# Performance work log

Measured on AMD Instinct MI355X. Metric: run time of the kernel, lower is better.

## Reference

```python
import jax, jax.numpy as jnp
import numpy as np
from jax.scipy.linalg import solve_triangular

EMB = 2048; NKH = 16; NVH = 32; DK = 128; DV = 128
KSZ = 4; EPS = 1e-6; CHUNK = 64
KEY_DIM = NKH * DK; VAL_DIM = NVH * DV
CONV_DIM = 2 * KEY_DIM + VAL_DIM  # q,k (key_dim each) + v (value_dim)
B, S = 1, 4096  # S % CHUNK == 0 -> no padding path


def setup_inputs() -> dict:
    key = jax.random.key(0)
    ks = jax.random.split(key, 7)
    s = 0.02
    return {
        "hidden_states": jax.random.normal(ks[0], (B, S, EMB), jnp.float32),
        "W_qkvz": jax.random.normal(ks[1], (EMB, 2 * KEY_DIM + 2 * VAL_DIM), jnp.float32) * s,
        "W_ba": jax.random.normal(ks[2], (EMB, 2 * NVH), jnp.float32) * s,
        "conv_kernel": jax.random.normal(ks[3], (KSZ, 1, CONV_DIM), jnp.float32) * 0.1,
        "A_log": jnp.log(jax.random.uniform(ks[4], (NVH,), jnp.float32, 1e-9, 16.0)),
        "dt_bias": jnp.ones((NVH,), jnp.float32),
        "norm_weight": jnp.ones((DV,), jnp.float32),
        "W_out": jax.random.normal(ks[5], (VAL_DIM, EMB), jnp.float32) * s,
    }


def _chunk_gated_delta_rule(q, k, v, g, beta):
    """q,k: [B,S,H,DK]; v: [B,S,H,DV]; g,beta: [B,S,H]. Returns [B,S,H,DV]."""
    dt = q.dtype
    prec = jax.lax.Precision.HIGHEST
    q = jnp.transpose(q, (0, 2, 1, 3)).astype(jnp.float32)
    k = jnp.transpose(k, (0, 2, 1, 3)).astype(jnp.float32)
    v = jnp.transpose(v, (0, 2, 1, 3)).astype(jnp.float32)
    beta = jnp.transpose(beta, (0, 2, 1)).astype(jnp.float32)
    g = jnp.transpose(g, (0, 2, 1)).astype(jnp.float32)
    b, h, s, dk = k.shape
    dv = v.shape[-1]
    nc = s // CHUNK
    q = q * jax.lax.rsqrt(jnp.float32(dk))
    v_beta = v * beta[..., None]
    k_beta = k * beta[..., None]
    qc = q.reshape(b, h, nc, CHUNK, dk)
    kc = k.reshape(b, h, nc, CHUNK, dk)
    kbc = k_beta.reshape(b, h, nc, CHUNK, dk)
    vbc = v_beta.reshape(b, h, nc, CHUNK, dv)
    gc = g.reshape(b, h, nc, CHUNK)
    g_cum = jnp.cumsum(gc, axis=-1)                        # [b,h,nc,C]
    g_diff = g_cum[..., :, None] - g_cum[..., None, :]     # [b,h,nc,C,C]
    decay = jnp.exp(jnp.tril(g_diff))
    tri_incl = jnp.triu(jnp.ones((CHUNK, CHUNK), bool), k=0)
    L = -jnp.matmul(kbc, jnp.swapaxes(kc, -1, -2), precision=prec) * decay
    L = jnp.where(tri_incl, 0.0, L)  # strictly lower
    eye = jnp.eye(CHUNK, dtype=jnp.float32)
    # UT transform: original fori_loop forward-substitution == (I - L)^{-1}
    attn = solve_triangular(eye - L, jnp.broadcast_to(eye, L.shape), lower=True)
    v_intra = jnp.matmul(attn, vbc, precision=prec)
    k_cumdecay = jnp.matmul(attn, kbc * jnp.exp(g_cum)[..., None], precision=prec)
    state0 = jnp.zeros((b, h, dk, dv), jnp.float32)
    tri_strict = jnp.triu(jnp.ones((CHUNK, CHUNK), bool), k=1)
    xs = tuple(jnp.moveaxis(t, 2, 0) for t in (qc, kc, v_intra, k_cumdecay, g_cum, decay))

    def scan_body(state, x):
        q_i, k_i, v_i, kcd_i, g_i, dm_i = x
        a_i = jnp.matmul(q_i, jnp.swapaxes(k_i, -1, -2), precision=prec) * dm_i
        a_i = jnp.where(tri_strict, 0.0, a_i)
        v_new = v_i - jnp.matmul(kcd_i, state, precision=prec)
        out_i = jnp.matmul(q_i * jnp.exp(g_i)[..., None], state, precision=prec) \
              + jnp.matmul(a_i, v_new, precision=prec)
        g_last = g_i[..., -1]
        new_state = state * jnp.exp(g_last)[..., None, None] \
            + jnp.matmul(jnp.swapaxes(k_i * jnp.exp(g_last[..., None] - g_i)[..., None], -1, -2),
                         v_new, precision=prec)
        return new_state, out_i

    _, out = jax.lax.scan(scan_body, state0, xs)
    out = jnp.moveaxis(out, 0, 2).reshape(b, h, s, dv)
    return jnp.transpose(out, (0, 2, 1, 3)).astype(dt)


def reference(hidden_states, W_qkvz, W_ba, conv_kernel, A_log, dt_bias, norm_weight, W_out):
    b, s, _ = hidden_states.shape
    vk = NVH // NKH  # v heads per k head
    qkvz = hidden_states @ W_qkvz                          # [b,s,12288]
    ba = hidden_states @ W_ba                              # [b,s,64]
    mixed = qkvz.reshape(b, s, NKH, 2 * DK + 2 * vk * DV)
    q, k, v_raw, z_raw = jnp.split(mixed, [DK, 2 * DK, 2 * DK + vk * DV], axis=3)
    value = v_raw.reshape(b, s, NVH, DV)
    z = z_raw.reshape(b, s, NVH, DV)
    mixed_ba = ba.reshape(b, s, NKH, 2 * vk)
    b_raw, a_raw = jnp.split(mixed_ba, [vk], axis=3)
    b_gate = b_raw.reshape(b, s, NVH)
    a_gate = a_raw.reshape(b, s, NVH)
    # depthwise causal conv over the concatenated q,k,v channels
    qkv = jnp.concatenate([q.reshape(b, s, -1), k.reshape(b, s, -1), value.reshape(b, s, -1)], axis=-1)
    x = jnp.pad(qkv, ((0, 0), (KSZ - 1, 0), (0, 0)))
    conv = jax.lax.conv_general_dilated(x, conv_kernel, (1,), 'VALID',
                                        dimension_numbers=('NWC', 'WIO', 'NWC'),
                                        feature_group_count=CONV_DIM)
    qkv_c = jax.nn.silu(conv.astype(jnp.float32)).astype(hidden_states.dtype)
    q_c, k_c, v_c = jnp.split(qkv_c, [KEY_DIM, 2 * KEY_DIM], axis=-1)
    query = q_c.reshape(b, s, NKH, DK)
    key = k_c.reshape(b, s, NKH, DK)
    value = v_c.reshape(b, s, NVH, DV)
    beta = jax.nn.sigmoid(b_gate)
    g = (-jnp.exp(A_log.astype(jnp.float32))
         * jax.nn.softplus(a_gate.astype(jnp.float32) + dt_bias.astype(jnp.float32))
         ).astype(hidden_states.dtype)
    query = jnp.repeat(query, vk, axis=2)
    key = jnp.repeat(key, vk, axis=2)
    core = _chunk_gated_delta_rule(query, key, value, g, beta)  # [b,s,NVH,DV]
    # gated RMSNorm (Mamba2-style): gate first, then normalize
    xf = core.astype(jnp.float32) * jax.nn.silu(z.astype(jnp.float32))
    var = jnp.mean(xf * xf, axis=-1, keepdims=True)
    xf = xf * jax.lax.rsqrt(var + EPS) * norm_weight
    out = xf.astype(hidden_states.dtype).reshape(b, s, VAL_DIM)
    return out @ W_out
```

## Files before the change

kernel.cpp:

```cpp
#include <hip/hip_runtime.h>


typedef __attribute__((ext_vector_type(8))) __bf16 bf16x8;
typedef __attribute__((ext_vector_type(4))) float f32x4;
typedef __bf16 bf16_t;

#define MFMA_BF16(A, B, C) __builtin_amdgcn_mfma_f32_16x16x32_bf16((A), (B), (C), 0, 0, 0)

__device__ __forceinline__ void async16(const bf16_t* g, bf16_t* l) {
  __builtin_amdgcn_global_load_lds(
      (const __attribute__((address_space(1))) unsigned*)g,
      (__attribute__((address_space(3))) unsigned*)l, 16, 0, 0);
}

__device__ __forceinline__ bf16_t f2bf(float x) {
  unsigned u = __builtin_bit_cast(unsigned, x);
  unsigned r = u + 0x7fffu + ((u >> 16) & 1u);
  unsigned short s = (unsigned short)(r >> 16);
  return __builtin_bit_cast(bf16_t, s);
}
__device__ __forceinline__ float bf2f(bf16_t b) {
  unsigned short s = __builtin_bit_cast(unsigned short, b);
  unsigned u = ((unsigned)s) << 16;
  return __builtin_bit_cast(float, u);
}
__device__ __forceinline__ unsigned packhl(float x) {
  bf16_t h = f2bf(x);
  bf16_t l = f2bf(x - bf2f(h));
  return (((unsigned)__builtin_bit_cast(unsigned short, h)) << 16) |
         (unsigned)__builtin_bit_cast(unsigned short, l);
}
__device__ __forceinline__ float upk(unsigned u) {
  return __builtin_bit_cast(float, u & 0xffff0000u) +
         __builtin_bit_cast(float, u << 16);
}

struct FragPair { bf16x8 hi, lo; };

__device__ __forceinline__ void load8(float v[8], const float* p) {
  float4 a = *(const float4*)p;
  float4 b = *(const float4*)(p + 4);
  v[0] = a.x; v[1] = a.y; v[2] = a.z; v[3] = a.w;
  v[4] = b.x; v[5] = b.y; v[6] = b.z; v[7] = b.w;
}
__device__ __forceinline__ void load8u(unsigned v[8], const unsigned* p) {
  uint4 a = *(const uint4*)p;
  uint4 b = *(const uint4*)(p + 4);
  v[0] = a.x; v[1] = a.y; v[2] = a.z; v[3] = a.w;
  v[4] = b.x; v[5] = b.y; v[6] = b.z; v[7] = b.w;
}
__device__ __forceinline__ FragPair split8(const float v[8]) {
  FragPair f;
#pragma unroll
  for (int j = 0; j < 8; j++) {
    bf16_t h = f2bf(v[j]);
    f.hi[j] = h;
    f.lo[j] = f2bf(v[j] - bf2f(h));
  }
  return f;
}
__device__ __forceinline__ FragPair unpack8(const unsigned v[8]) {
  FragPair f;
#pragma unroll
  for (int j = 0; j < 8; j++) {
    f.hi[j] = __builtin_bit_cast(bf16_t, (unsigned short)(v[j] >> 16));
    f.lo[j] = __builtin_bit_cast(bf16_t, (unsigned short)(v[j] & 0xffffu));
  }
  return f;
}

__global__ void k_cvt(const float* __restrict__ in, bf16_t* __restrict__ out, int n) {
  int i = (blockIdx.x * 256 + threadIdx.x) * 4;
  if (i + 3 < n) {
    float4 v = *(const float4*)(in + i);
    out[i + 0] = f2bf(v.x); out[i + 1] = f2bf(v.y);
    out[i + 2] = f2bf(v.z); out[i + 3] = f2bf(v.w);
  }
}

__global__ void k_transpose_cvt(const float* __restrict__ in, bf16_t* __restrict__ out,
                                int K, int N) {
  __shared__ bf16_t tile[64 * 65];
  int n0 = blockIdx.x * 64, k0 = blockIdx.y * 64;
  int c = threadIdx.x & 63, rg = threadIdx.x >> 6;
#pragma unroll
  for (int rr = 0; rr < 16; rr++) {
    int r = rr * 4 + rg;
    tile[c * 65 + r] = f2bf(in[(size_t)(k0 + r) * N + n0 + c]);
  }
  __syncthreads();
#pragma unroll
  for (int rr = 0; rr < 16; rr++) {
    int r = rr * 4 + rg;
    out[(size_t)(n0 + r) * K + k0 + c] = tile[r * 65 + c];
  }
}

__global__ void k_ktrans(const bf16_t* __restrict__ kb, bf16_t* __restrict__ kbT) {
  __shared__ __align__(16) bf16_t t[128][72];
  int kh = blockIdx.x >> 6, ci = blockIdx.x & 63, s0 = ci * 64;
  int s = threadIdx.x & 63, dg = threadIdx.x >> 6;
  const bf16_t* src = kb + (size_t)(s0 + s) * 2048 + kh * 128 + dg * 32;
#pragma unroll
  for (int j = 0; j < 4; j++) {
    bf16x8 v = *(const bf16x8*)(src + j * 8);
#pragma unroll
    for (int e = 0; e < 8; e++) t[dg * 32 + j * 8 + e][s] = v[e];
  }
  __syncthreads();
  int d = threadIdx.x >> 1, sh = (threadIdx.x & 1) * 32;
  bf16_t* dst = kbT + ((size_t)blockIdx.x * 128 + d) * 64 + sh;
#pragma unroll
  for (int j = 0; j < 4; j++)
    *(bf16x8*)(dst + j * 8) = *(const bf16x8*)(&t[d][sh + j * 8]);
}

__global__ __launch_bounds__(256) void k_gemm(const bf16_t* __restrict__ A,
                                              const bf16_t* __restrict__ BT,
                                              float* __restrict__ C, int M, int N, int K) {
  __shared__ __align__(16) bf16_t sA[128 * 32];
  __shared__ __align__(16) bf16_t sB[128 * 32];
  const int tid = threadIdx.x;
  const int lane = tid & 63, w = tid >> 6;
  const int quad = lane >> 4, l15 = lane & 15;
  const int m0 = blockIdx.y * 128, n0 = blockIdx.x * 128;
  const int wm = (w >> 1) * 64, wn = (w & 1) * 64;
  f32x4 acc[4][4];
#pragma unroll
  for (int a = 0; a < 4; a++)
#pragma unroll
    for (int b = 0; b < 4; b++) { f32x4 z = {0.f, 0.f, 0.f, 0.f}; acc[a][b] = z; }
  const int sb = (lane & 7) ^ ((lane >> 3) & 7);
  const int srow = ((tid >> 3) << 1) + (sb >> 2);
  const int scol = (sb & 3) * 8;
  const bf16_t* gA = A + (size_t)(m0 + srow) * K + scol;
  const bf16_t* gB = BT + (size_t)(n0 + srow) * K + scol;
  bf16_t* lA = sA + w * 512;
  bf16_t* lB = sB + w * 512;
  const int rh = l15 >> 1;
  const int bs = (((l15 & 1) << 2) + quad) ^ rh;
  const int foff = rh * 64 + bs * 8;
  for (int kt = 0; kt < K; kt += 32) {
    async16(gA + kt, lA);
    async16(gA + (size_t)64 * K + kt, lA + 2048);
    async16(gB + kt, lB);
    async16(gB + (size_t)64 * K + kt, lB + 2048);
    __syncthreads();
    bf16x8 af[4], bfv[4];
#pragma unroll
    for (int t = 0; t < 4; t++) {
      af[t]  = *(const bf16x8*)(sA + ((wm >> 1) + t * 8) * 64 + foff);
      bfv[t] = *(const bf16x8*)(sB + ((wn >> 1) + t * 8) * 64 + foff);
    }
#pragma unroll
    for (int mt = 0; mt < 4; mt++)
#pragma unroll
      for (int nt = 0; nt < 4; nt++)
        acc[mt][nt] = MFMA_BF16(af[mt], bfv[nt], acc[mt][nt]);
    __syncthreads();
  }
#pragma unroll
  for (int mt = 0; mt < 4; mt++)
#pragma unroll
    for (int nt = 0; nt < 4; nt++) {
      int row0 = m0 + wm + mt * 16 + quad * 4;
      int col = n0 + wn + nt * 16 + l15;
#pragma unroll
      for (int r = 0; r < 4; r++)
        C[(size_t)(row0 + r) * N + col] = acc[mt][nt][r];
    }
}

__global__ __launch_bounds__(512, 2) void k_gemm_qkvz(const bf16_t* __restrict__ A,
                                                      const bf16_t* __restrict__ BT,
                                                      bf16_t* __restrict__ qkvb,
                                                      bf16_t* __restrict__ zb,
                                                      int M, int N, int K) {
  __shared__ __align__(16) bf16_t sA[4 * 8192];
  __shared__ __align__(16) bf16_t sB[4 * 8192];
  const int tid = threadIdx.x;
  const int lane = tid & 63, w = tid >> 6;
  const int quad = lane >> 4, l15 = lane & 15;

  const int nwg = gridDim.x * gridDim.y;
  const int cpx = nwg >> 3;
  int id = blockIdx.y * gridDim.x + blockIdx.x;
  id = (id & 7) * cpx + (id >> 3);
  const int bx = id % gridDim.x, by = id / gridDim.x;
  const int m0 = by * 256, n0 = bx * 256;
  const int wm = (w >> 2) * 128, wn = (w & 3) * 64;

  f32x4 acc[8][4];
#pragma unroll
  for (int m = 0; m < 8; m++)
#pragma unroll
    for (int n = 0; n < 4; n++) { f32x4 z = {0.f, 0.f, 0.f, 0.f}; acc[m][n] = z; }

  const int srow = w * 16 + (lane >> 2);
  const int sq = (lane & 3) ^ ((lane >> 3) & 3);
  const bf16_t* gA = A + (size_t)(m0 + srow) * K + sq * 8;
  const bf16_t* gB = BT + (size_t)(n0 + srow) * K + sq * 8;
  const size_t rowskip = (size_t)128 * K;

  const int pblk = (quad ^ ((l15 >> 1) & 3)) << 3;
  const int fA = (wm + l15) * 32 + pblk;
  const int fB = (wn + l15) * 32 + pblk;

  const int NT = K >> 5;

  auto stage = [&](int t) {
    bf16_t* lA = sA + (t & 3) * 8192 + w * 512;
    bf16_t* lB = sB + (t & 3) * 8192 + w * 512;
    const bf16_t* pA = gA + t * 32;
    const bf16_t* pB = gB + t * 32;
    async16(pA, lA);
    async16(pA + rowskip, lA + 4096);
    async16(pB, lB);
    async16(pB + rowskip, lB + 4096);
  };

  if (0 < NT) stage(0);
  if (1 < NT) stage(1);
  if (2 < NT) stage(2);

  for (int t = 0; t < NT; ++t) {
    if (t + 3 < NT) stage(t + 3);
    const int ahead = NT - 1 - t;
    if (ahead >= 3)      asm volatile("s_waitcnt vmcnt(12)" ::: "memory");
    else if (ahead == 2) asm volatile("s_waitcnt vmcnt(8)" ::: "memory");
    else if (ahead == 1) asm volatile("s_waitcnt vmcnt(4)" ::: "memory");
    else                 asm volatile("s_waitcnt vmcnt(0)" ::: "memory");
    __builtin_amdgcn_s_barrier();
    asm volatile("" ::: "memory");
    __builtin_amdgcn_sched_barrier(0);

    const bf16_t* bA = sA + (t & 3) * 8192;
    const bf16_t* bB = sB + (t & 3) * 8192;
    bf16x8 af[8], bfv[4];
#pragma unroll
    for (int m = 0; m < 8; m++) af[m] = *(const bf16x8*)(bA + fA + m * 512);
#pragma unroll
    for (int n = 0; n < 4; n++) bfv[n] = *(const bf16x8*)(bB + fB + n * 512);

    __builtin_amdgcn_s_setprio(1);
#pragma unroll
    for (int m = 0; m < 8; m++)
#pragma unroll
      for (int n = 0; n < 4; n++)
        acc[m][n] = MFMA_BF16(af[m], bfv[n], acc[m][n]);
    __builtin_amdgcn_s_setprio(0);

    asm volatile("" ::: "memory");
    __builtin_amdgcn_sched_barrier(0);
    __builtin_amdgcn_s_barrier();
  }

#pragma unroll
  for (int n = 0; n < 4; n++) {
    int c = n0 + wn + n * 16 + l15;
    int kh = c / 768;
    int rr = c - kh * 768;
    bool isz = (rr >= 512);
    bf16_t* dst = isz ? zb : qkvb;
    size_t stride = isz ? 4096 : 8192;
    size_t coff = isz ? (size_t)(kh * 256 + (rr - 512)) : (size_t)(kh * 512 + rr);
#pragma unroll
    for (int m = 0; m < 8; m++) {
      int row0 = m0 + wm + m * 16 + quad * 4;
#pragma unroll
      for (int r = 0; r < 4; r++)
        dst[(size_t)(row0 + r) * stride + coff] = f2bf(acc[m][n][r]);
    }
  }
}

__global__ __launch_bounds__(256) void k_ba(const float* __restrict__ hs,
                                            const float* __restrict__ Wba,
                                            const float* __restrict__ A_log,
                                            const float* __restrict__ dtb,
                                            float* __restrict__ g, float* __restrict__ beta) {
  __shared__ float sH[4][2048];
  int s0 = blockIdx.x * 32;
  int c = threadIdx.x & 63, sg = threadIdx.x >> 6;
  for (int rg = 0; rg < 8; rg++) {
    __syncthreads();
    for (int i = threadIdx.x; i < 2048; i += 256) {
      int r = i >> 9, kk = (i & 511) * 4;
      *(float4*)(&sH[r][kk]) = *(const float4*)(hs + (size_t)(s0 + rg * 4 + r) * 2048 + kk);
    }
    __syncthreads();
    float dot = 0.f;
    for (int kk = 0; kk < 2048; kk += 4) {
      float4 hv = *(const float4*)(&sH[sg][kk]);
      dot += hv.x * Wba[(kk + 0) * 64 + c] + hv.y * Wba[(kk + 1) * 64 + c] +
             hv.z * Wba[(kk + 2) * 64 + c] + hv.w * Wba[(kk + 3) * 64 + c];
    }
    int s = s0 + rg * 4 + sg;
    int hh = c >> 2, j = c & 3;
    if (j < 2) {
      int vh = hh * 2 + j;
      beta[s * 32 + vh] = 1.f / (1.f + __expf(-dot));
    } else {
      int vh = hh * 2 + (j - 2);
      float x = dot + dtb[vh];
      float sp = (x > 20.f) ? x : log1pf(__expf(x));
      g[s * 32 + vh] = -__expf(A_log[vh]) * sp;
    }
  }
}

__global__ void k_conv(const bf16_t* __restrict__ qkvb, const float* __restrict__ ck,
                       bf16_t* __restrict__ qb, bf16_t* __restrict__ kb,
                       bf16_t* __restrict__ vb) {
  int c = blockIdx.x * 256 + threadIdx.x;
  int s0 = blockIdx.y * 128;
  int col, dstc, dstride;
  bf16_t* dst;
  float scale = 1.0f;
  if (c < 2048) {
    int hh = c >> 7, d = c & 127;
    col = hh * 512 + d; dst = qb; dstc = c; dstride = 2048;
    scale = 0.08838834764831845f;
  } else if (c < 4096) {
    int cc = c - 2048, hh = cc >> 7, d = cc & 127;
    col = hh * 512 + 128 + d; dst = kb; dstc = cc; dstride = 2048;
  } else {
    int cc = c - 4096, vh = cc >> 7, d = cc & 127;
    col = (vh >> 1) * 512 + 256 + (vh & 1) * 128 + d; dst = vb; dstc = cc; dstride = 4096;
  }
  float w0 = ck[c], w1 = ck[8192 + c], w2 = ck[2 * 8192 + c], w3 = ck[3 * 8192 + c];
  float x0 = 0.f, x1 = 0.f, x2 = 0.f;
  if (s0 >= 3) {
    x0 = bf2f(qkvb[(size_t)(s0 - 3) * 8192 + col]);
    x1 = bf2f(qkvb[(size_t)(s0 - 2) * 8192 + col]);
    x2 = bf2f(qkvb[(size_t)(s0 - 1) * 8192 + col]);
  }
  for (int s = s0; s < s0 + 128; s++) {
    float x3 = bf2f(qkvb[(size_t)s * 8192 + col]);
    float y = w0 * x0 + w1 * x1 + w2 * x2 + w3 * x3;
    y = y / (1.f + __expf(-y));
    dst[(size_t)s * dstride + dstc] = f2bf(y * scale);
    x0 = x1; x1 = x2; x2 = x3;
  }
}

__global__ __launch_bounds__(256) void k_phaseA(const bf16_t* __restrict__ kb,
                                                const bf16_t* __restrict__ vb,
                                                const float* __restrict__ g,
                                                const float* __restrict__ beta,
                                                float* __restrict__ vi,
                                                bf16_t* __restrict__ kcdn) {
  __shared__ __align__(16) char smem[36608];
  float* sGc = (float*)smem;
  float* sBt = (float*)(smem + 256);
  float* sBE = (float*)(smem + 512);
  float* sP  = (float*)(smem + 768);
  bf16_t* sQ  = (bf16_t*)(smem + 18176);
  bf16_t* sQT = (bf16_t*)(smem + 27392);
  bf16_t* sVT = (bf16_t*)(smem + 18176);
  bf16_t* sKT = (bf16_t*)(smem + 27392);

  const int tid = threadIdx.x, lane = tid & 63, w = tid >> 6;
  const int quad = lane >> 4, l15 = lane & 15;
  const int h = blockIdx.x >> 6, ci = blockIdx.x & 63;
  const int kh = h >> 1, s0 = ci * 64;
  const int m = w * 16 + l15;

  if (tid < 64) {
    float gv = g[(size_t)(s0 + tid) * 32 + h];
    float bv = beta[(size_t)(s0 + tid) * 32 + h];
#pragma unroll
    for (int off = 1; off < 64; off <<= 1) {
      float t = __shfl_up(gv, off, 64);
      if (tid >= off) gv += t;
    }
    sGc[tid] = gv; sBt[tid] = bv; sBE[tid] = bv * __expf(gv);
  }
  __syncthreads();

  const bf16_t* krow = kb + (size_t)s0 * 2048 + kh * 128;
  bf16x8 ak[4];
#pragma unroll
  for (int ks = 0; ks < 4; ks++)
    ak[ks] = *(const bf16x8*)(krow + (size_t)m * 2048 + ks * 32 + quad * 8);
  f32x4 accL[4];
#pragma unroll
  for (int nt = 0; nt < 4; nt++) { f32x4 z = {0.f, 0.f, 0.f, 0.f}; accL[nt] = z; }
#pragma unroll
  for (int nt = 0; nt < 4; nt++)
#pragma unroll
    for (int ks = 0; ks < 4; ks++) {
      bf16x8 bk = *(const bf16x8*)(krow + (size_t)(nt * 16 + l15) * 2048 + ks * 32 + quad * 8);
      accL[nt] = MFMA_BF16(ak[ks], bk, accL[nt]);
    }
#pragma unroll
  for (int nt = 0; nt < 4; nt++) {
    int j = nt * 16 + l15;
#pragma unroll
    for (int r = 0; r < 4; r++) {
      int i = w * 16 + quad * 4 + r;
      float Lij = (i > j) ? (-accL[nt][r] * sBt[i] * __expf(sGc[i] - sGc[j])) : 0.f;
      sP[i * 68 + j] = ((i == j) ? 1.f : 0.f) + Lij;
      bf16_t q16 = f2bf(Lij);
      sQ[i * 72 + j] = q16;
      sQT[j * 72 + i] = q16;
    }
  }
  __syncthreads();

  for (int it = 0; it < 5; it++) {
    f32x4 accQ[4];
#pragma unroll
    for (int nt = 0; nt < 4; nt++) { f32x4 z = {0.f, 0.f, 0.f, 0.f}; accQ[nt] = z; }
    bf16x8 qa[2];
#pragma unroll
    for (int ks = 0; ks < 2; ks++)
      qa[ks] = *(const bf16x8*)(sQ + m * 72 + ks * 32 + quad * 8);
#pragma unroll
    for (int nt = 0; nt < 4; nt++)
#pragma unroll
      for (int ks = 0; ks < 2; ks++) {
        bf16x8 qv = *(const bf16x8*)(sQT + (nt * 16 + l15) * 72 + ks * 32 + quad * 8);
        accQ[nt] = MFMA_BF16(qa[ks], qv, accQ[nt]);
      }
    __syncthreads();
#pragma unroll
    for (int nt = 0; nt < 4; nt++) {
      int j = nt * 16 + l15;
#pragma unroll
      for (int r = 0; r < 4; r++) {
        int i = w * 16 + quad * 4 + r;
        bf16_t q16 = f2bf(accQ[nt][r]);
        sQ[i * 72 + j] = q16;
        sQT[j * 72 + i] = q16;
      }
    }
    __syncthreads();
    f32x4 accP[4];
#pragma unroll
    for (int nt = 0; nt < 4; nt++) { f32x4 z = {0.f, 0.f, 0.f, 0.f}; accP[nt] = z; }
    FragPair pa[2];
#pragma unroll
    for (int ks = 0; ks < 2; ks++) {
      float v[8];
      load8(v, sP + m * 68 + ks * 32 + quad * 8);
      pa[ks] = split8(v);
    }
#pragma unroll
    for (int nt = 0; nt < 4; nt++)
#pragma unroll
      for (int ks = 0; ks < 2; ks++) {
        bf16x8 qv = *(const bf16x8*)(sQT + (nt * 16 + l15) * 72 + ks * 32 + quad * 8);
        accP[nt] = MFMA_BF16(pa[ks].hi, qv, accP[nt]);
        accP[nt] = MFMA_BF16(pa[ks].lo, qv, accP[nt]);
      }
#pragma unroll
    for (int nt = 0; nt < 4; nt++) {
      int j = nt * 16 + l15;
#pragma unroll
      for (int r = 0; r < 4; r++) {
        int i = w * 16 + quad * 4 + r;
        sP[i * 68 + j] += accP[nt][r];
      }
    }
  }

  FragPair paV[2], paK[2];
#pragma unroll
  for (int ks = 0; ks < 2; ks++) {
    float v[8];
    load8(v, sP + m * 68 + ks * 32 + quad * 8);
    float vv[8], vk[8];
#pragma unroll
    for (int jj = 0; jj < 8; jj++) {
      int i = ks * 32 + quad * 8 + jj;
      vv[jj] = v[jj] * sBt[i];
      vk[jj] = v[jj] * sBE[i];
    }
    paV[ks] = split8(vv);
    paK[ks] = split8(vk);
  }

  for (int hf = 0; hf < 2; hf++) {
    __syncthreads();
    {
      int sidx = tid & 63, dg = tid >> 6;
      const bf16_t* vsrc = vb + (size_t)(s0 + sidx) * 4096 + h * 128 + hf * 64 + dg * 16;
      const bf16_t* ksrc = kb + (size_t)(s0 + sidx) * 2048 + kh * 128 + hf * 64 + dg * 16;
      bf16x8 v0 = *(const bf16x8*)vsrc;
      bf16x8 v1 = *(const bf16x8*)(vsrc + 8);
      bf16x8 k0 = *(const bf16x8*)ksrc;
      bf16x8 k1 = *(const bf16x8*)(ksrc + 8);
#pragma unroll
      for (int e = 0; e < 8; e++) {
        sVT[(dg * 16 + e) * 72 + sidx] = v0[e];
        sVT[(dg * 16 + 8 + e) * 72 + sidx] = v1[e];
        sKT[(dg * 16 + e) * 72 + sidx] = k0[e];
        sKT[(dg * 16 + 8 + e) * 72 + sidx] = k1[e];
      }
    }
    __syncthreads();
    f32x4 accV[4], accK[4];
#pragma unroll
    for (int nt = 0; nt < 4; nt++) {
      f32x4 z = {0.f, 0.f, 0.f, 0.f};
      accV[nt] = z; accK[nt] = z;
    }
#pragma unroll
    for (int nt = 0; nt < 4; nt++)
#pragma unroll
      for (int ks = 0; ks < 2; ks++) {
        bf16x8 bv = *(const bf16x8*)(sVT + (nt * 16 + l15) * 72 + ks * 32 + quad * 8);
        accV[nt] = MFMA_BF16(paV[ks].hi, bv, accV[nt]);
        accV[nt] = MFMA_BF16(paV[ks].lo, bv, accV[nt]);
        bf16x8 bk = *(const bf16x8*)(sKT + (nt * 16 + l15) * 72 + ks * 32 + quad * 8);
        accK[nt] = MFMA_BF16(paK[ks].hi, bk, accK[nt]);
        accK[nt] = MFMA_BF16(paK[ks].lo, bk, accK[nt]);
      }
#pragma unroll
    for (int nt = 0; nt < 4; nt++) {
      int col = hf * 64 + nt * 16 + l15;
#pragma unroll
      for (int r = 0; r < 4; r++) {
        int row = w * 16 + quad * 4 + r;
        size_t o = ((size_t)h * 4096 + s0 + row) * 128 + col;
        vi[o] = accV[nt][r];
        kcdn[o] = f2bf(-accK[nt][r]);
      }
    }
  }
}

__global__ __launch_bounds__(256) void k_phaseB(const bf16_t* __restrict__ qb,
                                                const bf16_t* __restrict__ kbT,
                                                const float* __restrict__ g,
                                                const float* __restrict__ vi,
                                                const bf16_t* __restrict__ kcdn,
                                                bf16_t* __restrict__ vnT,
                                                bf16_t* __restrict__ outp) {
  __shared__ __align__(16) char smem[13312];
  float* sGc2 = (float*)smem;
  unsigned* sSTp = (unsigned*)(smem + 512);
  unsigned* sVTp = (unsigned*)(smem + 8960);
  const int tid = threadIdx.x, lane = tid & 63, w = tid >> 6;
  const int quad = lane >> 4, l15 = lane & 15;
  const int h = blockIdx.x >> 3, cg = blockIdx.x & 7;
  const int kh = h >> 1, col0 = cg * 16;
  const int m = w * 16 + l15;

  for (int i = tid; i < 16 * 132; i += 256) sSTp[i] = 0u;
  if (tid < 64) {
    float gv = g[(size_t)tid * 32 + h];
#pragma unroll
    for (int off = 1; off < 64; off <<= 1) {
      float t = __shfl_up(gv, off, 64);
      if (tid >= off) gv += t;
    }
    sGc2[tid] = gv;
  }
  __syncthreads();

  for (int ci = 0; ci < 64; ci++) {
    const int s0 = ci * 64;
    const float* sGc = sGc2 + (ci & 1) * 64;

    const bf16_t* kcrow = kcdn + ((size_t)h * 4096 + s0 + m) * 128;
    const bf16_t* qrow = qb + (size_t)(s0 + m) * 2048 + kh * 128;
    bf16x8 a1[4], a2[4], kT[2][2];
#pragma unroll
    for (int d = 0; d < 4; d++) {
      a1[d] = *(const bf16x8*)(kcrow + d * 32 + quad * 8);
      a2[d] = *(const bf16x8*)(qrow + d * 32 + quad * 8);
    }
#pragma unroll
    for (int mi = 0; mi < 2; mi++)
#pragma unroll
      for (int ks = 0; ks < 2; ks++)
        kT[mi][ks] = *(const bf16x8*)(kbT + ((size_t)(kh * 64 + ci) * 128 +
                                             w * 32 + mi * 16 + l15) * 64 + ks * 32 + quad * 8);
    const int colg = col0 + l15;
    size_t vbase = ((size_t)h * 4096 + s0 + w * 16 + quad * 4) * 128 + colg;
    f32x4 accV = {vi[vbase], vi[vbase + 128], vi[vbase + 256], vi[vbase + 384]};
    f32x4 accO = {0.f, 0.f, 0.f, 0.f};
#pragma unroll
    for (int d = 0; d < 4; d++) {
      unsigned u[8];
      load8u(u, sSTp + l15 * 132 + d * 32 + quad * 8);
      FragPair B = unpack8(u);
      accV = MFMA_BF16(a1[d], B.hi, accV);
      accV = MFMA_BF16(a1[d], B.lo, accV);
      accO = MFMA_BF16(a2[d], B.hi, accO);
      accO = MFMA_BF16(a2[d], B.lo, accO);
    }
    const float gl = sGc[63];
    {
      bf16_t* vout = vnT + ((size_t)(h * 64 + ci) * 128 + colg) * 64 + w * 16 + quad * 4;
      bf16_t* oout = outp + vbase;
      ushort4 vv;
      unsigned pk[4];
      unsigned short vb_[4];
#pragma unroll
      for (int r = 0; r < 4; r++) {
        float gr = sGc[w * 16 + quad * 4 + r];
        oout[(size_t)r * 128] = f2bf(accO[r] * __expf(gr));
        vb_[r] = __builtin_bit_cast(unsigned short, f2bf(accV[r]));
        pk[r] = packhl(accV[r] * __expf(gl - gr));
      }
      vv.x = vb_[0]; vv.y = vb_[1]; vv.z = vb_[2]; vv.w = vb_[3];
      *(ushort4*)vout = vv;
      uint4 pv; pv.x = pk[0]; pv.y = pk[1]; pv.z = pk[2]; pv.w = pk[3];
      *(uint4*)(sVTp + l15 * 68 + w * 16 + quad * 4) = pv;
    }
    __syncthreads();

    f32x4 accD[2];
#pragma unroll
    for (int mi = 0; mi < 2; mi++) { f32x4 z = {0.f, 0.f, 0.f, 0.f}; accD[mi] = z; }
#pragma unroll
    for (int ks = 0; ks < 2; ks++) {
      unsigned u[8];
      load8u(u, sVTp + l15 * 68 + ks * 32 + quad * 8);
      FragPair Bv = unpack8(u);
#pragma unroll
      for (int mi = 0; mi < 2; mi++) {
        accD[mi] = MFMA_BF16(kT[mi][ks], Bv.hi, accD[mi]);
        accD[mi] = MFMA_BF16(kT[mi][ks], Bv.lo, accD[mi]);
      }
    }
    float egl = __expf(gl);
#pragma unroll
    for (int mi = 0; mi < 2; mi++) {
      int row0 = w * 32 + mi * 16 + quad * 4;
      unsigned* ps = sSTp + l15 * 132 + row0;
      uint4 old4 = *(uint4*)ps;
      uint4 nu;
      nu.x = packhl(upk(old4.x) * egl + accD[mi][0]);
      nu.y = packhl(upk(old4.y) * egl + accD[mi][1]);
      nu.z = packhl(upk(old4.z) * egl + accD[mi][2]);
      nu.w = packhl(upk(old4.w) * egl + accD[mi][3]);
      *(uint4*)ps = nu;
    }
    if (ci + 1 < 64 && tid < 64) {
      float gv = g[(size_t)((ci + 1) * 64 + tid) * 32 + h];
#pragma unroll
      for (int off = 1; off < 64; off <<= 1) {
        float t = __shfl_up(gv, off, 64);
        if (tid >= off) gv += t;
      }
      sGc2[((ci + 1) & 1) * 64 + tid] = gv;
    }
    __syncthreads();
  }
}

__global__ __launch_bounds__(256) void k_phaseC(const bf16_t* __restrict__ qb,
                                                const bf16_t* __restrict__ kb,
                                                const float* __restrict__ g,
                                                const bf16_t* __restrict__ vnT,
                                                const bf16_t* __restrict__ outp,
                                                const bf16_t* __restrict__ zb,
                                                const float* __restrict__ nw,
                                                bf16_t* __restrict__ xf) {
  __shared__ __align__(16) char smem[17664];
  float* sGc = (float*)smem;
  unsigned* sAp = (unsigned*)(smem + 256);
  const int tid = threadIdx.x, lane = tid & 63, w = tid >> 6;
  const int quad = lane >> 4, l15 = lane & 15;
  const int h = blockIdx.x >> 6, ci = blockIdx.x & 63;
  const int kh = h >> 1, s0 = ci * 64;
  const int m = w * 16 + l15;

  if (tid < 64) {
    float gv = g[(size_t)(s0 + tid) * 32 + h];
#pragma unroll
    for (int off = 1; off < 64; off <<= 1) {
      float t = __shfl_up(gv, off, 64);
      if (tid >= off) gv += t;
    }
    sGc[tid] = gv;
  }
  __syncthreads();

  const bf16_t* qrow = qb + (size_t)s0 * 2048 + kh * 128;
  const bf16_t* krow = kb + (size_t)s0 * 2048 + kh * 128;
  bf16x8 aq[4];
#pragma unroll
  for (int ks = 0; ks < 4; ks++)
    aq[ks] = *(const bf16x8*)(qrow + (size_t)m * 2048 + ks * 32 + quad * 8);
  f32x4 accA[4];
#pragma unroll
  for (int nt = 0; nt < 4; nt++) { f32x4 z = {0.f, 0.f, 0.f, 0.f}; accA[nt] = z; }
#pragma unroll
  for (int nt = 0; nt < 4; nt++)
#pragma unroll
    for (int ks = 0; ks < 4; ks++) {
      bf16x8 bk = *(const bf16x8*)(krow + (size_t)(nt * 16 + l15) * 2048 + ks * 32 + quad * 8);
      accA[nt] = MFMA_BF16(aq[ks], bk, accA[nt]);
    }
#pragma unroll
  for (int nt = 0; nt < 4; nt++) {
    int j = nt * 16 + l15;
#pragma unroll
    for (int r = 0; r < 4; r++) {
      int i = w * 16 + quad * 4 + r;
      float a = (i >= j) ? accA[nt][r] * __expf(sGc[i] - sGc[j]) : 0.f;
      sAp[i * 68 + j] = packhl(a);
    }
  }
  __syncthreads();

  FragPair Aa[2];
#pragma unroll
  for (int ks = 0; ks < 2; ks++) {
    unsigned u[8];
    load8u(u, sAp + m * 68 + ks * 32 + quad * 8);
    Aa[ks] = unpack8(u);
  }
  f32x4 accO[8];
#pragma unroll
  for (int nt = 0; nt < 8; nt++) {
    size_t base = ((size_t)h * 4096 + s0 + w * 16 + quad * 4) * 128 + nt * 16 + l15;
    f32x4 z;
    z[0] = bf2f(outp[base]); z[1] = bf2f(outp[base + 128]);
    z[2] = bf2f(outp[base + 256]); z[3] = bf2f(outp[base + 384]);
    accO[nt] = z;
  }
#pragma unroll
  for (int nt = 0; nt < 8; nt++)
#pragma unroll
    for (int ks = 0; ks < 2; ks++) {
      bf16x8 bv = *(const bf16x8*)(vnT + ((size_t)(h * 64 + ci) * 128 + nt * 16 + l15) * 64 +
                                   ks * 32 + quad * 8);
      accO[nt] = MFMA_BF16(Aa[ks].hi, bv, accO[nt]);
      accO[nt] = MFMA_BF16(Aa[ks].lo, bv, accO[nt]);
    }

  float xv[8][4];
  float ss[4] = {0.f, 0.f, 0.f, 0.f};
#pragma unroll
  for (int nt = 0; nt < 8; nt++) {
    int dv = nt * 16 + l15;
#pragma unroll
    for (int r = 0; r < 4; r++) {
      int s = s0 + w * 16 + quad * 4 + r;
      float z = bf2f(zb[(size_t)s * 4096 + h * 128 + dv]);
      float gate = z / (1.f + __expf(-z));
      float val = accO[nt][r] * gate;
      xv[nt][r] = val;
      ss[r] += val * val;
    }
  }
#pragma unroll
  for (int off = 1; off < 16; off <<= 1) {
#pragma unroll
    for (int r = 0; r < 4; r++) ss[r] += __shfl_xor(ss[r], off, 64);
  }
  float rs[4];
#pragma unroll
  for (int r = 0; r < 4; r++) rs[r] = rsqrtf(ss[r] * (1.f / 128.f) + 1e-6f);
#pragma unroll
  for (int nt = 0; nt < 8; nt++) {
    int dv = nt * 16 + l15;
    float nwv = nw[dv];
#pragma unroll
    for (int r = 0; r < 4; r++) {
      int s = s0 + w * 16 + quad * 4 + r;
      xf[(size_t)s * 4096 + h * 128 + dv] = f2bf(xv[nt][r] * rs[r] * nwv);
    }
  }
}

extern "C" void kernel_launch(void* const* d_in, const int* in_sizes, int n_in,
                              void* d_out, int out_size, void* d_ws, size_t ws_size,
                              hipStream_t stream) {
  const float* hs = (const float*)d_in[0];
  const float* Wqkvz = (const float*)d_in[1];
  const float* Wba = (const float*)d_in[2];
  const float* convk = (const float*)d_in[3];
  const float* A_log = (const float*)d_in[4];
  const float* dtb = (const float*)d_in[5];
  const float* nw = (const float*)d_in[6];
  const float* Wout = (const float*)d_in[7];
  float* out = (float*)d_out;
  char* ws = (char*)d_ws;

  const size_t NEED = 252706816u;
  if (ws_size < NEED) return;

  bf16_t* hsbf = (bf16_t*)(ws + 0);
  bf16_t* wqkT = (bf16_t*)(ws + 16777216);
  bf16_t* qb   = (bf16_t*)(ws + 0);
  bf16_t* kb   = (bf16_t*)(ws + 16777216);
  bf16_t* vb   = (bf16_t*)(ws + 33554432);
  bf16_t* vnT  = (bf16_t*)(ws + 33554432);
  bf16_t* qkvb = (bf16_t*)(ws + 67108864);
  float*  vi   = (float*)(ws + 67108864);
  bf16_t* xf   = (bf16_t*)(ws + 67108864);
  bf16_t* zb   = (bf16_t*)(ws + 134217728);
  float*  gbuf = (float*)(ws + 167772160);
  float*  bbuf = (float*)(ws + 168296448);
  bf16_t* kcdn = (bf16_t*)(ws + 168820736);
  bf16_t* woutT= (bf16_t*)(ws + 168820736);
  bf16_t* outp = (bf16_t*)(ws + 202375168);
  bf16_t* kbT  = (bf16_t*)(ws + 235929600);

  k_cvt<<<8192, 256, 0, stream>>>(hs, hsbf, 4096 * 2048);
  k_transpose_cvt<<<dim3(192, 32), 256, 0, stream>>>(Wqkvz, wqkT, 2048, 12288);
  k_gemm_qkvz<<<dim3(48, 16), 512, 0, stream>>>(hsbf, wqkT, qkvb, zb,
                                                4096, 12288, 2048);
  k_ba<<<128, 256, 0, stream>>>(hs, Wba, A_log, dtb, gbuf, bbuf);
  k_conv<<<dim3(32, 32), 256, 0, stream>>>(qkvb, convk, qb, kb, vb);
  k_ktrans<<<1024, 256, 0, stream>>>(kb, kbT);
  k_phaseA<<<2048, 256, 0, stream>>>(kb, vb, gbuf, bbuf, vi, kcdn);
  k_phaseB<<<256, 256, 0, stream>>>(qb, kbT, gbuf, vi, kcdn, vnT, outp);
  k_phaseC<<<2048, 256, 0, stream>>>(qb, kb, gbuf, vnT, outp, zb, nw, xf);
  k_transpose_cvt<<<dim3(32, 64), 256, 0, stream>>>(Wout, woutT, 4096, 2048);
  k_gemm<<<dim3(16, 32), 256, 0, stream>>>(xf, woutT, out, 4096, 2048, 4096);
}
```

Baseline: 1.094 ms.

## Split QKVZ GEMM K-step into two half-phases interleaving LDS reads, async loads, MFMAs

Restructures the main loop of the QKVZ projection GEMM so each K-step is split into two halves. Each half issues LDS fragment reads and part of the next stage's global-to-LDS loads, then runs half the MFMAs, with barriers between phases. The aim is to overlap memory traffic with MFMA work and ease register pressure. It also replaces the generic XCD-chunked block remap with a fixed mapping that assumes 6 N-tiles per XCD, which hardcodes the grid shape.

Result: faster. 1.039 ms (-5.0%).

```diff
diff --git a/kernel.cpp b/kernel.cpp
--- a/kernel.cpp
+++ b/kernel.cpp
@@ -182,11 +182,9 @@
   const int lane = tid & 63, w = tid >> 6;
   const int quad = lane >> 4, l15 = lane & 15;
 
-  const int nwg = gridDim.x * gridDim.y;
-  const int cpx = nwg >> 3;
   int id = blockIdx.y * gridDim.x + blockIdx.x;
-  id = (id & 7) * cpx + (id >> 3);
-  const int bx = id % gridDim.x, by = id / gridDim.x;
+  const int xcd = id & 7, jj = id >> 3;
+  const int bx = xcd * 6 + (jj % 6), by = jj / 6;
   const int m0 = by * 256, n0 = bx * 256;
   const int wm = (w >> 2) * 128, wn = (w & 3) * 64;
 
@@ -208,49 +206,66 @@
 
   const int NT = K >> 5;
 
-  auto stage = [&](int t) {
-    bf16_t* lA = sA + (t & 3) * 8192 + w * 512;
-    bf16_t* lB = sB + (t & 3) * 8192 + w * 512;
+  for (int t = 0; t < 3; ++t) {
+    bf16_t* lA = sA + t * 8192 + w * 512;
+    bf16_t* lB = sB + t * 8192 + w * 512;
     const bf16_t* pA = gA + t * 32;
     const bf16_t* pB = gB + t * 32;
     async16(pA, lA);
     async16(pA + rowskip, lA + 4096);
     async16(pB, lB);
     async16(pB + rowskip, lB + 4096);
-  };
-
-  if (0 < NT) stage(0);
-  if (1 < NT) stage(1);
-  if (2 < NT) stage(2);
+  }
+  asm volatile("s_waitcnt vmcnt(8)" ::: "memory");
+  __builtin_amdgcn_s_barrier();
 
   for (int t = 0; t < NT; ++t) {
-    if (t + 3 < NT) stage(t + 3);
-    const int ahead = NT - 1 - t;
-    if (ahead >= 3)      asm volatile("s_waitcnt vmcnt(12)" ::: "memory");
-    else if (ahead == 2) asm volatile("s_waitcnt vmcnt(8)" ::: "memory");
-    else if (ahead == 1) asm volatile("s_waitcnt vmcnt(4)" ::: "memory");
-    else                 asm volatile("s_waitcnt vmcnt(0)" ::: "memory");
+    const bf16_t* bAs = sA + (t & 3) * 8192;
+    const bf16_t* bBs = sB + (t & 3) * 8192;
+    bf16_t* lA = sA + ((t + 3) & 3) * 8192 + w * 512;
+    bf16_t* lB = sB + ((t + 3) & 3) * 8192 + w * 512;
+    const bf16_t* pA = gA + (size_t)(t + 3) * 32;
+    const bf16_t* pB = gB + (size_t)(t + 3) * 32;
+    const bool st = (t + 3) < NT;
+
+    bf16x8 af0[4], af1[4], bfv[4];
+
+#pragma unroll
+    for (int mm = 0; mm < 4; mm++) af0[mm] = *(const bf16x8*)(bAs + fA + mm * 512);
+#pragma unroll
+    for (int nn = 0; nn < 4; nn++) bfv[nn] = *(const bf16x8*)(bBs + fB + nn * 512);
+    if (st) { async16(pA, lA); async16(pA + rowskip, lA + 4096); }
+    __builtin_amdgcn_sched_barrier(0);
     __builtin_amdgcn_s_barrier();
-    asm volatile("" ::: "memory");
+    asm volatile("s_waitcnt lgkmcnt(0)" ::: "memory");
     __builtin_amdgcn_sched_barrier(0);
-
-    const bf16_t* bA = sA + (t & 3) * 8192;
-    const bf16_t* bB = sB + (t & 3) * 8192;
-    bf16x8 af[8], bfv[4];
-#pragma unroll
-    for (int m = 0; m < 8; m++) af[m] = *(const bf16x8*)(bA + fA + m * 512);
-#pragma unroll
-    for (int n = 0; n < 4; n++) bfv[n] = *(const bf16x8*)(bB + fB + n * 512);
-
     __builtin_amdgcn_s_setprio(1);
 #pragma unroll
-    for (int m = 0; m < 8; m++)
-#pragma unroll
-      for (int n = 0; n < 4; n++)
-        acc[m][n] = MFMA_BF16(af[m], bfv[n], acc[m][n]);
+    for (int mm = 0; mm < 4; mm++)
+#pragma unroll
+      for (int nn = 0; nn < 4; nn++)
+        acc[mm][nn] = MFMA_BF16(af0[mm], bfv[nn], acc[mm][nn]);
     __builtin_amdgcn_s_setprio(0);
-
-    asm volatile("" ::: "memory");
+    __builtin_amdgcn_sched_barrier(0);
+    __builtin_amdgcn_s_barrier();
+
+#pragma unroll
+    for (int mm = 0; mm < 4; mm++) af1[mm] = *(const bf16x8*)(bAs + fA + (4 + mm) * 512);
+    if (st) { async16(pB, lB); async16(pB + rowskip, lB + 4096); }
+    if (t + 3 < NT)      asm volatile("s_waitcnt vmcnt(8)" ::: "memory");
+    else if (t + 2 < NT) asm volatile("s_waitcnt vmcnt(4)" ::: "memory");
+    else if (t + 1 < NT) asm volatile("s_waitcnt vmcnt(0)" ::: "memory");
+    __builtin_amdgcn_sched_barrier(0);
+    __builtin_amdgcn_s_barrier();
+    asm volatile("s_waitcnt lgkmcnt(0)" ::: "memory");
+    __builtin_amdgcn_sched_barrier(0);
+    __builtin_amdgcn_s_setprio(1);
+#pragma unroll
+    for (int mm = 0; mm < 4; mm++)
+#pragma unroll
+      for (int nn = 0; nn < 4; nn++)
+        acc[4 + mm][nn] = MFMA_BF16(af1[mm], bfv[nn], acc[4 + mm][nn]);
+    __builtin_amdgcn_s_setprio(0);
     __builtin_amdgcn_sched_barrier(0);
     __builtin_amdgcn_s_barrier();
   }
```

## Restructure qkvz GEMM into 8-phase ping-pong pipeline with 64-wide K tiles

Applied to the files above, without the earlier changes.

Rewrites the main loop of the qkvz projection GEMM. K tiles grow from 32 to 64 and sit in a two-buffer LDS layout split into A and B halves. Each iteration is broken into barrier-separated phases that interleave LDS fragment loads, async global-to-LDS staging and MFMA sub-blocks, so loads overlap compute at a finer grain. It also swaps the generic XCD-aware block remap for a hardcoded XCD grouping that assumes 6 column tiles per XCD. The cost is many more barriers and hand-tuned waitcnt values that depend on the grid shape.

After: 1.022 ms. 1.07x faster.

```diff
diff --git a/kernel.cpp b/kernel.cpp
--- a/kernel.cpp
+++ b/kernel.cpp
@@ -176,19 +176,19 @@
                                                       bf16_t* __restrict__ qkvb,
                                                       bf16_t* __restrict__ zb,
                                                       int M, int N, int K) {
-  __shared__ __align__(16) bf16_t sA[4 * 8192];
-  __shared__ __align__(16) bf16_t sB[4 * 8192];
+  __shared__ __align__(16) bf16_t sL[2 * 4 * 8192];
   const int tid = threadIdx.x;
   const int lane = tid & 63, w = tid >> 6;
   const int quad = lane >> 4, l15 = lane & 15;
 
-  const int nwg = gridDim.x * gridDim.y;
-  const int cpx = nwg >> 3;
   int id = blockIdx.y * gridDim.x + blockIdx.x;
-  id = (id & 7) * cpx + (id >> 3);
-  const int bx = id % gridDim.x, by = id / gridDim.x;
+  const int xcd = id & 7, jj = id >> 3;
+  const int bx = xcd * 6 + (jj % 6), by = jj / 6;
   const int m0 = by * 256, n0 = bx * 256;
   const int wm = (w >> 2) * 128, wn = (w & 3) * 64;
+  const int hA = (w >> 2);
+  const int hB = 2 + ((w & 3) >> 1);
+  const int brow0 = wn & 64;
 
   f32x4 acc[8][4];
 #pragma unroll
@@ -196,64 +196,115 @@
 #pragma unroll
     for (int n = 0; n < 4; n++) { f32x4 z = {0.f, 0.f, 0.f, 0.f}; acc[m][n] = z; }
 
-  const int srow = w * 16 + (lane >> 2);
-  const int sq = (lane & 3) ^ ((lane >> 3) & 3);
-  const bf16_t* gA = A + (size_t)(m0 + srow) * K + sq * 8;
-  const bf16_t* gB = BT + (size_t)(n0 + srow) * K + sq * 8;
-  const size_t rowskip = (size_t)128 * K;
-
-  const int pblk = (quad ^ ((l15 >> 1) & 3)) << 3;
-  const int fA = (wm + l15) * 32 + pblk;
-  const int fB = (wn + l15) * 32 + pblk;
-
-  const int NT = K >> 5;
-
-  auto stage = [&](int t) {
-    bf16_t* lA = sA + (t & 3) * 8192 + w * 512;
-    bf16_t* lB = sB + (t & 3) * 8192 + w * 512;
-    const bf16_t* pA = gA + t * 32;
-    const bf16_t* pB = gB + t * 32;
-    async16(pA, lA);
-    async16(pA + rowskip, lA + 4096);
-    async16(pB, lB);
-    async16(pB + rowskip, lB + 4096);
+  const int rbase = w * 8 + (lane >> 3);
+  const int sq = (lane & 7) ^ ((lane >> 3) & 7);
+  const bf16_t* gb[4];
+  gb[0] = A + (size_t)(m0 + rbase) * K + sq * 8;
+  gb[1] = A + (size_t)(m0 + 128 + rbase) * K + sq * 8;
+  gb[2] = BT + (size_t)(n0 + rbase) * K + sq * 8;
+  gb[3] = BT + (size_t)(n0 + 128 + rbase) * K + sq * 8;
+  const size_t j64 = (size_t)64 * K;
+
+  bf16x8 afr[4][2], bf01[2][2], bf23[2][2];
+  const int NI = K >> 7;
+
+  auto stg = [&](int cb, int h, int kt) {
+    const bf16_t* s = gb[h] + (size_t)kt * 64;
+    bf16_t* d = sL + (cb * 4 + h) * 8192 + w * 512;
+    async16(s, d);
+    async16(s + j64, d + 4096);
   };
-
-  if (0 < NT) stage(0);
-  if (1 < NT) stage(1);
-  if (2 < NT) stage(2);
-
-  for (int t = 0; t < NT; ++t) {
-    if (t + 3 < NT) stage(t + 3);
-    const int ahead = NT - 1 - t;
-    if (ahead >= 3)      asm volatile("s_waitcnt vmcnt(12)" ::: "memory");
-    else if (ahead == 2) asm volatile("s_waitcnt vmcnt(8)" ::: "memory");
-    else if (ahead == 1) asm volatile("s_waitcnt vmcnt(4)" ::: "memory");
-    else                 asm volatile("s_waitcnt vmcnt(0)" ::: "memory");
-    __builtin_amdgcn_s_barrier();
-    asm volatile("" ::: "memory");
-    __builtin_amdgcn_sched_barrier(0);
-
-    const bf16_t* bA = sA + (t & 3) * 8192;
-    const bf16_t* bB = sB + (t & 3) * 8192;
-    bf16x8 af[8], bfv[4];
-#pragma unroll
-    for (int m = 0; m < 8; m++) af[m] = *(const bf16x8*)(bA + fA + m * 512);
-#pragma unroll
-    for (int n = 0; n < 4; n++) bfv[n] = *(const bf16x8*)(bB + fB + n * 512);
-
+  auto ldA = [&](int cb, int mg) {
+    const bf16_t* base = sL + (cb * 4 + hA) * 8192;
+#pragma unroll
+    for (int m = 0; m < 4; m++)
+#pragma unroll
+      for (int ks = 0; ks < 2; ks++)
+        afr[m][ks] = *(const bf16x8*)(base + (mg * 64 + m * 16 + l15) * 64 +
+                                      (((ks * 4 + quad) ^ (l15 & 7)) * 8));
+  };
+  auto ldB = [&](int cb, int ng, bf16x8 (&bf)[2][2]) {
+    const bf16_t* base = sL + (cb * 4 + hB) * 8192;
+#pragma unroll
+    for (int n = 0; n < 2; n++)
+#pragma unroll
+      for (int ks = 0; ks < 2; ks++)
+        bf[n][ks] = *(const bf16x8*)(base + (brow0 + ng * 32 + n * 16 + l15) * 64 +
+                                     (((ks * 4 + quad) ^ (l15 & 7)) * 8));
+  };
+  auto mm = [&](int mg, int ng, bf16x8 (&bf)[2][2]) {
     __builtin_amdgcn_s_setprio(1);
 #pragma unroll
-    for (int m = 0; m < 8; m++)
-#pragma unroll
-      for (int n = 0; n < 4; n++)
-        acc[m][n] = MFMA_BF16(af[m], bfv[n], acc[m][n]);
+    for (int m = 0; m < 4; m++)
+#pragma unroll
+      for (int n = 0; n < 2; n++)
+#pragma unroll
+        for (int ks = 0; ks < 2; ks++)
+          acc[mg * 4 + m][ng * 2 + n] =
+              MFMA_BF16(afr[m][ks], bf[n][ks], acc[mg * 4 + m][ng * 2 + n]);
     __builtin_amdgcn_s_setprio(0);
-
-    asm volatile("" ::: "memory");
-    __builtin_amdgcn_sched_barrier(0);
-    __builtin_amdgcn_s_barrier();
-  }
+  };
+
+#define PH_OPEN()                                           \
+  do {                                                      \
+    __builtin_amdgcn_sched_barrier(0);                      \
+    __builtin_amdgcn_s_barrier();                           \
+    asm volatile("s_waitcnt lgkmcnt(0)" ::: "memory");      \
+    __builtin_amdgcn_sched_barrier(0);                      \
+  } while (0)
+#define PH_CLOSE()                                          \
+  do {                                                      \
+    __builtin_amdgcn_sched_barrier(0);                      \
+    __builtin_amdgcn_s_barrier();                           \
+  } while (0)
+
+#pragma unroll
+  for (int h = 0; h < 4; h++) stg(0, h, 0);
+  stg(1, 2, 1);
+  stg(1, 3, 1);
+  asm volatile("s_waitcnt vmcnt(4)" ::: "memory");
+  __builtin_amdgcn_s_barrier();
+
+  for (int i = 0; i < NI; ++i) {
+    const int k2 = 2 * i;
+    const bool more = (i + 1 < NI);
+    ldA(0, 0); ldB(0, 0, bf01);
+    stg(1, 0, k2 + 1);
+    asm volatile("s_waitcnt lgkmcnt(8)" ::: "memory");
+    PH_OPEN(); mm(0, 0, bf01); PH_CLOSE();
+    ldB(0, 1, bf23);
+    stg(1, 1, k2 + 1);
+    PH_OPEN(); mm(0, 1, bf23); PH_CLOSE();
+    ldA(0, 1);
+    if (more) stg(0, 2, k2 + 2);
+    PH_OPEN(); mm(1, 0, bf01); PH_CLOSE();
+    if (more) {
+      stg(0, 3, k2 + 2);
+      asm volatile("s_waitcnt vmcnt(4)" ::: "memory");
+    } else {
+      asm volatile("s_waitcnt vmcnt(0)" ::: "memory");
+    }
+    PH_OPEN(); mm(1, 1, bf23); PH_CLOSE();
+    ldA(1, 0); ldB(1, 0, bf01);
+    if (more) stg(0, 0, k2 + 2);
+    asm volatile("s_waitcnt lgkmcnt(8)" ::: "memory");
+    PH_OPEN(); mm(0, 0, bf01); PH_CLOSE();
+    ldB(1, 1, bf23);
+    if (more) stg(0, 1, k2 + 2);
+    PH_OPEN(); mm(0, 1, bf23); PH_CLOSE();
+    ldA(1, 1);
+    if (more) stg(1, 2, k2 + 3);
+    PH_OPEN(); mm(1, 0, bf01); PH_CLOSE();
+    if (more) {
+      stg(1, 3, k2 + 3);
+      asm volatile("s_waitcnt vmcnt(4)" ::: "memory");
+    } else {
+      asm volatile("s_waitcnt vmcnt(0)" ::: "memory");
+    }
+    PH_OPEN(); mm(1, 1, bf23); PH_CLOSE();
+  }
+#undef PH_OPEN
+#undef PH_CLOSE
 
 #pragma unroll
   for (int n = 0; n < 4; n++) {
```
